# Performance work log

Hardware: AMD Instinct MI355X
Metric: run time of the kernel (lower is better)

## Reference

```python
import jax, jax.numpy as jnp
import numpy as np

N_NODES = 50000
N_EDGES = 800000
IN_DIM = 128
HIDDEN = 128
NUM_CLASSES = 2
NUM_GRAPHS = 512


def _linear_params(key, fan_in, fan_out):
    # torch nn.Linear default init: U(-1/sqrt(fan_in), 1/sqrt(fan_in))
    k1, k2 = jax.random.split(key)
    bound = 1.0 / np.sqrt(fan_in)
    W = jax.random.uniform(k1, (fan_in, fan_out), jnp.float32, -bound, bound)
    b = jax.random.uniform(k2, (fan_out,), jnp.float32, -bound, bound)
    return W, b


def setup_inputs() -> dict:
    key = jax.random.key(0)
    ks = jax.random.split(key, 8)
    x = jax.random.normal(ks[0], (N_NODES, IN_DIM), jnp.float32)
    edge_index = jax.random.randint(ks[1], (2, N_EDGES), 0, N_NODES, jnp.int64)
    batch = jnp.sort(jax.random.randint(ks[2], (N_NODES,), 0, NUM_GRAPHS, jnp.int64))
    W1a, b1a = _linear_params(ks[3], IN_DIM, HIDDEN)
    W1b, b1b = _linear_params(ks[4], HIDDEN, HIDDEN)
    W2a, b2a = _linear_params(ks[5], HIDDEN, HIDDEN)
    W2b, b2b = _linear_params(ks[6], HIDDEN, HIDDEN)
    Wfc, bfc = _linear_params(ks[7], HIDDEN, NUM_CLASSES)
    return {"x": x, "edge_index": edge_index, "batch": batch,
            "W1a": W1a, "b1a": b1a, "W1b": W1b, "b1b": b1b,
            "W2a": W2a, "b2a": b2a, "W2b": W2b, "b2b": b2b,
            "Wfc": Wfc, "bfc": bfc}


def _gin_layer(x, src, dst, Wa, ba, Wb, bb):
    # GINConv (eps=0): h_i = MLP(x_i + sum_{j->i} x_j)
    agg = jax.ops.segment_sum(x[src], dst, num_segments=N_NODES)
    h = x + agg
    h = jax.nn.relu(h @ Wa + ba)
    h = h @ Wb + bb
    return jax.nn.relu(h)  # outer F.relu in forward; dropout is identity (eval)


def reference(x, edge_index, batch, W1a, b1a, W1b, b1b, W2a, b2a, W2b, b2b, Wfc, bfc):
    src, dst = edge_index[0], edge_index[1]
    h = _gin_layer(x, src, dst, W1a, b1a, W1b, b1b)
    h = _gin_layer(h, src, dst, W2a, b2a, W2b, b2b)
    # global mean pool per graph
    sums = jax.ops.segment_sum(h, batch, num_segments=NUM_GRAPHS)
    counts = jax.ops.segment_sum(jnp.ones((N_NODES,), h.dtype), batch, num_segments=NUM_GRAPHS)
    g_emb = sums / jnp.maximum(counts, 1.0)[:, None]
    return g_emb @ Wfc + bfc  # [NUM_GRAPHS, NUM_CLASSES]
```

## Files before the change

kernel.cpp:

```cpp
#include <hip/hip_runtime.h>

typedef unsigned short ushort_t;
typedef unsigned int uint_t;

typedef __bf16 bf16x8 __attribute__((ext_vector_type(8)));
typedef float f32x4 __attribute__((ext_vector_type(4)));

#define N_NODES 50000
#define N_EDGES 800000
#define DIM 128
#define NUM_GRAPHS 512
#define LDA 136

#define ELL_CAP 64

#define EDGE_BLOCKS ((N_EDGES + 255) / 256)
#define PREP_X_BLOCKS 6250
#define PREP_W_BLOCKS 256
#define PREP_B_BLOCKS 196
#define PREP_TOTAL (EDGE_BLOCKS + PREP_X_BLOCKS + PREP_W_BLOCKS + PREP_B_BLOCKS + 1)

__device__ __forceinline__ float bf2f(ushort_t u) {
    return __uint_as_float(((uint_t)u) << 16);
}
__device__ __forceinline__ ushort_t f2bf(float f) {
    uint_t u = __float_as_uint(f);
    u = (u + 0x7FFF + ((u >> 16) & 1)) >> 16;
    return (ushort_t)u;
}
__device__ __forceinline__ bf16x8 as_bf16x8(uint4 v) {
    return __builtin_bit_cast(bf16x8, v);
}

__global__ void zero_detect_kernel(int* cnt, float* gsum, const void* xraw,
                                   const void* eiraw, int* flags) {
    int i = blockIdx.x * 256 + threadIdx.x;
    if (i < N_NODES) cnt[i] = 0;
    if (i < NUM_GRAPHS * DIM) gsum[i] = 0.f;
    if (i == 0) {
        const ushort_t* u = (const ushort_t*)xraw;
        int extreme = 0;
        for (int k = 0; k < 128; ++k) {
            int e = (u[k] >> 7) & 0xFF;
            if (e >= 0xC0) extreme++;
        }
        flags[0] = (extreme > 8) ? 1 : 0;
        const int* p = (const int*)eiraw;
        int nonzero = 0;
        for (int k = 1; k < 64; k += 2) nonzero += (p[k] != 0);
        flags[1] = (nonzero == 0) ? 1 : 0;
    }
}

__global__ __launch_bounds__(256) void prep_all_kernel(
    const void* xraw, const void* braw, const void* eiraw,
    const void* W0, const void* W1, const void* W2, const void* W3,
    const void* pb1a, const void* pb1b, const void* pb2a, const void* pb2b,
    const void* pWfc, const void* pbfc, const int* __restrict__ flags,
    ushort_t* __restrict__ xout, ushort_t* __restrict__ wpout,
    int* __restrict__ batch32, float* __restrict__ params,
    int* __restrict__ cnt, int* __restrict__ ell) {
    int b = blockIdx.x;
    int tid = threadIdx.x;
    if (b < EDGE_BLOCKS) {
        int e = b * 256 + tid;
        if (e < N_EDGES) {
            const int* p = (const int*)eiraw;
            int s, d;
            if (flags[1]) {
                s = p[2 * e];
                d = p[2 * (N_EDGES + e)];
            } else {
                s = p[e];
                d = p[N_EDGES + e];
            }
            int slot = atomicAdd(&cnt[d], 1);
            if (slot < ELL_CAP) ell[d * ELL_CAP + slot] = s;
        }
    } else if (b < EDGE_BLOCKS + PREP_X_BLOCKS) {
        int i = (b - EDGE_BLOCKS) * 256 + tid;
        if (i < N_NODES * DIM / 4) {
            if (flags[0]) {
                float4 v = ((const float4*)xraw)[i];
                ushort4 o;
                o.x = f2bf(v.x); o.y = f2bf(v.y); o.z = f2bf(v.z); o.w = f2bf(v.w);
                ((ushort4*)xout)[i] = o;
            } else {
                ((uint2*)xout)[i] = ((const uint2*)xraw)[i];
            }
        }
    } else if (b < EDGE_BLOCKS + PREP_X_BLOCKS + PREP_W_BLOCKS) {
        int gidx = (b - EDGE_BLOCKS - PREP_X_BLOCKS) * 256 + tid;
        int which = gidx >> 14;
        const void* W = (which == 0) ? W0 : (which == 1) ? W1 : (which == 2) ? W2 : W3;
        int idx = gidx & 16383;
        int j = idx & 7;
        int L = (idx >> 3) & 63;
        int t = (idx >> 9) & 7;
        int s = idx >> 12;
        int k = s * 32 + (L >> 4) * 8 + j;
        int n = t * 16 + (L & 15);
        int off = k * DIM + n;
        wpout[gidx] = flags[0] ? f2bf(((const float*)W)[off]) : ((const ushort_t*)W)[off];
    } else if (b < EDGE_BLOCKS + PREP_X_BLOCKS + PREP_W_BLOCKS + PREP_B_BLOCKS) {
        int i = (b - EDGE_BLOCKS - PREP_X_BLOCKS - PREP_W_BLOCKS) * 256 + tid;
        if (i < N_NODES) {
            const int* p = (const int*)braw;
            batch32[i] = flags[1] ? p[2 * i] : p[i];
        }
    } else {
        for (int i = tid; i < 770; i += 256) {
            const void* srcp;
            int j;
            if (i < 128)      { srcp = pb1a; j = i; }
            else if (i < 256) { srcp = pb1b; j = i - 128; }
            else if (i < 384) { srcp = pb2a; j = i - 256; }
            else if (i < 512) { srcp = pb2b; j = i - 384; }
            else if (i < 768) { srcp = pWfc; j = i - 512; }
            else              { srcp = pbfc; j = i - 768; }
            params[i] = flags[0] ? ((const float*)srcp)[j] : bf2f(((const ushort_t*)srcp)[j]);
        }
    }
}

__global__ __launch_bounds__(256) void agg_kernel(const ushort_t* __restrict__ feat,
                                                  const int* __restrict__ deg,
                                                  const int* __restrict__ ell,
                                                  ushort_t* __restrict__ hout) {
    int n = blockIdx.x * 16 + (threadIdx.x >> 4);
    int lane = threadIdx.x & 15;
    if (n >= N_NODES) return;
    const uint4* fp = reinterpret_cast<const uint4*>(feat);
    uint4 v = fp[(size_t)n * 16 + lane];
    float a0 = bf2f((ushort_t)(v.x & 0xffff));
    float a1 = bf2f((ushort_t)(v.x >> 16));
    float a2 = bf2f((ushort_t)(v.y & 0xffff));
    float a3 = bf2f((ushort_t)(v.y >> 16));
    float a4 = bf2f((ushort_t)(v.z & 0xffff));
    float a5 = bf2f((ushort_t)(v.z >> 16));
    float a6 = bf2f((ushort_t)(v.w & 0xffff));
    float a7 = bf2f((ushort_t)(v.w >> 16));
    int e1 = deg[n];
    if (e1 > ELL_CAP) e1 = ELL_CAP;
    const int* __restrict__ row = ell + (size_t)n * ELL_CAP;
    int j = 0;
#define ACC8(V) \
    a0 += bf2f((ushort_t)((V).x & 0xffff)); a1 += bf2f((ushort_t)((V).x >> 16)); \
    a2 += bf2f((ushort_t)((V).y & 0xffff)); a3 += bf2f((ushort_t)((V).y >> 16)); \
    a4 += bf2f((ushort_t)((V).z & 0xffff)); a5 += bf2f((ushort_t)((V).z >> 16)); \
    a6 += bf2f((ushort_t)((V).w & 0xffff)); a7 += bf2f((ushort_t)((V).w >> 16));
    for (; j + 8 <= e1; j += 8) {
        int s0 = row[j],     s1 = row[j + 1], s2 = row[j + 2], s3 = row[j + 3];
        int s4 = row[j + 4], s5 = row[j + 5], s6 = row[j + 6], s7 = row[j + 7];
        uint4 g0 = fp[(size_t)s0 * 16 + lane];
        uint4 g1 = fp[(size_t)s1 * 16 + lane];
        uint4 g2 = fp[(size_t)s2 * 16 + lane];
        uint4 g3 = fp[(size_t)s3 * 16 + lane];
        uint4 g4 = fp[(size_t)s4 * 16 + lane];
        uint4 g5 = fp[(size_t)s5 * 16 + lane];
        uint4 g6 = fp[(size_t)s6 * 16 + lane];
        uint4 g7 = fp[(size_t)s7 * 16 + lane];
        ACC8(g0) ACC8(g1) ACC8(g2) ACC8(g3)
        ACC8(g4) ACC8(g5) ACC8(g6) ACC8(g7)
    }
    for (; j + 4 <= e1; j += 4) {
        int s0 = row[j], s1 = row[j + 1], s2 = row[j + 2], s3 = row[j + 3];
        uint4 g0 = fp[(size_t)s0 * 16 + lane];
        uint4 g1 = fp[(size_t)s1 * 16 + lane];
        uint4 g2 = fp[(size_t)s2 * 16 + lane];
        uint4 g3 = fp[(size_t)s3 * 16 + lane];
        ACC8(g0) ACC8(g1) ACC8(g2) ACC8(g3)
    }
    for (; j < e1; ++j) {
        int s = row[j];
        uint4 g0 = fp[(size_t)s * 16 + lane];
        ACC8(g0)
    }
#undef ACC8
    uint4 o;
    o.x = (uint_t)f2bf(a0) | ((uint_t)f2bf(a1) << 16);
    o.y = (uint_t)f2bf(a2) | ((uint_t)f2bf(a3) << 16);
    o.z = (uint_t)f2bf(a4) | ((uint_t)f2bf(a5) << 16);
    o.w = (uint_t)f2bf(a6) | ((uint_t)f2bf(a7) << 16);
    reinterpret_cast<uint4*>(hout)[(size_t)n * 16 + lane] = o;
}

__global__ __launch_bounds__(256) void mlp_kernel(const ushort_t* __restrict__ hin,
                                                  const ushort_t* __restrict__ wpA,
                                                  const float* __restrict__ ba,
                                                  const ushort_t* __restrict__ wpB,
                                                  const float* __restrict__ bb,
                                                  ushort_t* __restrict__ hout) {
    __shared__ ushort_t As[64 * LDA];
    int tid = threadIdx.x;
    int wave = tid >> 6;
    int lane = tid & 63;
    int quad = lane >> 4;
    int cl = lane & 15;
    int row0 = blockIdx.x * 64;

    bf16x8 B1[2][4], B2[2][4];
#pragma unroll
    for (int ti = 0; ti < 2; ++ti) {
        int t = 2 * wave + ti;
#pragma unroll
        for (int s = 0; s < 4; ++s) {
            B1[ti][s] = as_bf16x8(reinterpret_cast<const uint4*>(wpA)[(s * 8 + t) * 64 + lane]);
            B2[ti][s] = as_bf16x8(reinterpret_cast<const uint4*>(wpB)[(s * 8 + t) * 64 + lane]);
        }
    }

    for (int i = tid; i < 64 * 16; i += 256) {
        int r = i >> 4, c8 = i & 15;
        uint4 v = make_uint4(0u, 0u, 0u, 0u);
        int gr = row0 + r;
        if (gr < N_NODES)
            v = reinterpret_cast<const uint4*>(hin + (size_t)gr * DIM)[c8];
        *reinterpret_cast<uint4*>(&As[r * LDA + c8 * 8]) = v;
    }
    __syncthreads();

    f32x4 acc[4][2];
#pragma unroll
    for (int m = 0; m < 4; ++m)
#pragma unroll
        for (int ti = 0; ti < 2; ++ti)
#pragma unroll
            for (int r = 0; r < 4; ++r) acc[m][ti][r] = 0.f;

#pragma unroll
    for (int s = 0; s < 4; ++s) {
#pragma unroll
        for (int m = 0; m < 4; ++m) {
            bf16x8 a = *reinterpret_cast<const bf16x8*>(&As[(m * 16 + cl) * LDA + s * 32 + quad * 8]);
#pragma unroll
            for (int ti = 0; ti < 2; ++ti)
                acc[m][ti] = __builtin_amdgcn_mfma_f32_16x16x32_bf16(a, B1[ti][s], acc[m][ti], 0, 0, 0);
        }
    }
    __syncthreads();

#pragma unroll
    for (int ti = 0; ti < 2; ++ti) {
        int col = 32 * wave + ti * 16 + cl;
        float bv = ba[col];
#pragma unroll
        for (int m = 0; m < 4; ++m)
#pragma unroll
            for (int r = 0; r < 4; ++r) {
                float v = acc[m][ti][r] + bv;
                As[(m * 16 + quad * 4 + r) * LDA + col] = f2bf(fmaxf(v, 0.f));
            }
    }
    __syncthreads();

#pragma unroll
    for (int m = 0; m < 4; ++m)
#pragma unroll
        for (int ti = 0; ti < 2; ++ti)
#pragma unroll
            for (int r = 0; r < 4; ++r) acc[m][ti][r] = 0.f;

#pragma unroll
    for (int s = 0; s < 4; ++s) {
#pragma unroll
        for (int m = 0; m < 4; ++m) {
            bf16x8 a = *reinterpret_cast<const bf16x8*>(&As[(m * 16 + cl) * LDA + s * 32 + quad * 8]);
#pragma unroll
            for (int ti = 0; ti < 2; ++ti)
                acc[m][ti] = __builtin_amdgcn_mfma_f32_16x16x32_bf16(a, B2[ti][s], acc[m][ti], 0, 0, 0);
        }
    }

#pragma unroll
    for (int ti = 0; ti < 2; ++ti) {
        int col = 32 * wave + ti * 16 + cl;
        float bv = bb[col];
#pragma unroll
        for (int m = 0; m < 4; ++m)
#pragma unroll
            for (int r = 0; r < 4; ++r) {
                int gr = row0 + m * 16 + quad * 4 + r;
                if (gr < N_NODES) {
                    float v = acc[m][ti][r] + bv;
                    hout[(size_t)gr * DIM + col] = f2bf(fmaxf(v, 0.f));
                }
            }
    }
}

__global__ __launch_bounds__(256) void mlp_pool_kernel(const ushort_t* __restrict__ hin,
                                                       const ushort_t* __restrict__ wpA,
                                                       const float* __restrict__ ba,
                                                       const ushort_t* __restrict__ wpB,
                                                       const float* __restrict__ bb,
                                                       const int* __restrict__ batch32,
                                                       float* __restrict__ gsum) {
    __shared__ ushort_t As[64 * LDA];
    int tid = threadIdx.x;
    int wave = tid >> 6;
    int lane = tid & 63;
    int quad = lane >> 4;
    int cl = lane & 15;
    int row0 = blockIdx.x * 64;

    bf16x8 B1[2][4], B2[2][4];
#pragma unroll
    for (int ti = 0; ti < 2; ++ti) {
        int t = 2 * wave + ti;
#pragma unroll
        for (int s = 0; s < 4; ++s) {
            B1[ti][s] = as_bf16x8(reinterpret_cast<const uint4*>(wpA)[(s * 8 + t) * 64 + lane]);
            B2[ti][s] = as_bf16x8(reinterpret_cast<const uint4*>(wpB)[(s * 8 + t) * 64 + lane]);
        }
    }

    for (int i = tid; i < 64 * 16; i += 256) {
        int r = i >> 4, c8 = i & 15;
        uint4 v = make_uint4(0u, 0u, 0u, 0u);
        int gr = row0 + r;
        if (gr < N_NODES)
            v = reinterpret_cast<const uint4*>(hin + (size_t)gr * DIM)[c8];
        *reinterpret_cast<uint4*>(&As[r * LDA + c8 * 8]) = v;
    }
    __syncthreads();

    f32x4 acc[4][2];
#pragma unroll
    for (int m = 0; m < 4; ++m)
#pragma unroll
        for (int ti = 0; ti < 2; ++ti)
#pragma unroll
            for (int r = 0; r < 4; ++r) acc[m][ti][r] = 0.f;

#pragma unroll
    for (int s = 0; s < 4; ++s) {
#pragma unroll
        for (int m = 0; m < 4; ++m) {
            bf16x8 a = *reinterpret_cast<const bf16x8*>(&As[(m * 16 + cl) * LDA + s * 32 + quad * 8]);
#pragma unroll
            for (int ti = 0; ti < 2; ++ti)
                acc[m][ti] = __builtin_amdgcn_mfma_f32_16x16x32_bf16(a, B1[ti][s], acc[m][ti], 0, 0, 0);
        }
    }
    __syncthreads();

#pragma unroll
    for (int ti = 0; ti < 2; ++ti) {
        int col = 32 * wave + ti * 16 + cl;
        float bv = ba[col];
#pragma unroll
        for (int m = 0; m < 4; ++m)
#pragma unroll
            for (int r = 0; r < 4; ++r) {
                float v = acc[m][ti][r] + bv;
                As[(m * 16 + quad * 4 + r) * LDA + col] = f2bf(fmaxf(v, 0.f));
            }
    }
    __syncthreads();

#pragma unroll
    for (int m = 0; m < 4; ++m)
#pragma unroll
        for (int ti = 0; ti < 2; ++ti)
#pragma unroll
            for (int r = 0; r < 4; ++r) acc[m][ti][r] = 0.f;

#pragma unroll
    for (int s = 0; s < 4; ++s) {
#pragma unroll
        for (int m = 0; m < 4; ++m) {
            bf16x8 a = *reinterpret_cast<const bf16x8*>(&As[(m * 16 + cl) * LDA + s * 32 + quad * 8]);
#pragma unroll
            for (int ti = 0; ti < 2; ++ti)
                acc[m][ti] = __builtin_amdgcn_mfma_f32_16x16x32_bf16(a, B2[ti][s], acc[m][ti], 0, 0, 0);
        }
    }
    __syncthreads();

#pragma unroll
    for (int ti = 0; ti < 2; ++ti) {
        int col = 32 * wave + ti * 16 + cl;
        float bv = bb[col];
#pragma unroll
        for (int m = 0; m < 4; ++m)
#pragma unroll
            for (int r = 0; r < 4; ++r) {
                float v = acc[m][ti][r] + bv;
                As[(m * 16 + quad * 4 + r) * LDA + col] = f2bf(fmaxf(v, 0.f));
            }
    }
    __syncthreads();

    int c = tid & 127;
    int rbase = (tid >> 7) * 32;
    float accp = 0.f;
    int curg = -1;
    for (int r = rbase; r < rbase + 32; ++r) {
        int gr = row0 + r;
        if (gr >= N_NODES) break;
        int g = batch32[gr];
        if (g != curg) {
            if (curg >= 0) atomicAdd(&gsum[curg * DIM + c], accp);
            curg = g;
            accp = 0.f;
        }
        accp += bf2f(As[r * LDA + c]);
    }
    if (curg >= 0) atomicAdd(&gsum[curg * DIM + c], accp);
}

__global__ __launch_bounds__(64) void fc_kernel(const float* __restrict__ gsum,
                                                const int* __restrict__ batch,
                                                const float* __restrict__ params,
                                                const int* __restrict__ flags,
                                                void* __restrict__ out) {
    int g = blockIdx.x;
    int l = threadIdx.x;
    int lo = 0, hi = N_NODES;
    while (lo < hi) { int mid = (lo + hi) >> 1; if (batch[mid] < g) lo = mid + 1; else hi = mid; }
    int start = lo;
    hi = N_NODES;
    while (lo < hi) { int mid = (lo + hi) >> 1; if (batch[mid] < g + 1) lo = mid + 1; else hi = mid; }
    int cnt = lo - start;
    float inv = 1.0f / (float)(cnt > 0 ? cnt : 1);
    float m0 = gsum[g * DIM + l] * inv;
    float m1 = gsum[g * DIM + 64 + l] * inv;
    float p0 = m0 * params[512 + l * 2 + 0] + m1 * params[512 + (64 + l) * 2 + 0];
    float p1 = m0 * params[512 + l * 2 + 1] + m1 * params[512 + (64 + l) * 2 + 1];
#pragma unroll
    for (int off = 32; off > 0; off >>= 1) {
        p0 += __shfl_down(p0, off, 64);
        p1 += __shfl_down(p1, off, 64);
    }
    if (l == 0) {
        float o0 = p0 + params[768];
        float o1 = p1 + params[769];
        if (flags[0]) {
            ((float*)out)[g * 2 + 0] = o0;
            ((float*)out)[g * 2 + 1] = o1;
        } else {
            ((ushort_t*)out)[g * 2 + 0] = f2bf(o0);
            ((ushort_t*)out)[g * 2 + 1] = f2bf(o1);
        }
    }
}

extern "C" void kernel_launch(void* const* d_in, const int* in_sizes, int n_in,
                              void* d_out, int out_size, void* d_ws, size_t ws_size,
                              hipStream_t stream) {
    const void* x = d_in[0];
    const void* ei = d_in[1];
    const void* batch = d_in[2];
    const void* W1a = d_in[3];
    const void* b1a = d_in[4];
    const void* W1b = d_in[5];
    const void* b1b = d_in[6];
    const void* W2a = d_in[7];
    const void* b2a = d_in[8];
    const void* W2b = d_in[9];
    const void* b2b = d_in[10];
    const void* Wfc = d_in[11];
    const void* bfc = d_in[12];

    char* base = (char*)d_ws;
    ushort_t* hX = (ushort_t*)base;   base += (size_t)N_NODES * DIM * 2;
    ushort_t* hA = (ushort_t*)base;   base += (size_t)N_NODES * DIM * 2;
    int* ell = (int*)base;            base += (size_t)N_NODES * ELL_CAP * 4;
    int* cnt = (int*)base;            base += (size_t)N_NODES * 4;
    int* batch32 = (int*)base;        base += (size_t)N_NODES * 4;
    ushort_t* wp = (ushort_t*)base;   base += 4 * 16384 * 2;
    float* params = (float*)base;     base += 772 * 4;
    float* gsum = (float*)base;       base += (size_t)NUM_GRAPHS * DIM * 4;
    int* flags = (int*)base;          base += 16;

    ushort_t* wpA1 = wp;
    ushort_t* wpB1 = wp + 16384;
    ushort_t* wpA2 = wp + 2 * 16384;
    ushort_t* wpB2 = wp + 3 * 16384;

    zero_detect_kernel<<<256, 256, 0, stream>>>(cnt, gsum, x, ei, flags);
    prep_all_kernel<<<PREP_TOTAL, 256, 0, stream>>>(x, batch, ei, W1a, W1b, W2a, W2b,
                                                    b1a, b1b, b2a, b2b, Wfc, bfc, flags,
                                                    hX, wp, batch32, params, cnt, ell);

    agg_kernel<<<(N_NODES + 15) / 16, 256, 0, stream>>>(hX, cnt, ell, hA);
    mlp_kernel<<<(N_NODES + 63) / 64, 256, 0, stream>>>(hA, wpA1, params + 0, wpB1, params + 128, hA);
    agg_kernel<<<(N_NODES + 15) / 16, 256, 0, stream>>>(hA, cnt, ell, hX);
    mlp_pool_kernel<<<(N_NODES + 63) / 64, 256, 0, stream>>>(hX, wpA2, params + 256, wpB2, params + 384,
                                                             batch32, gsum);
    fc_kernel<<<NUM_GRAPHS, 64, 0, stream>>>(gsum, batch32, params, flags, d_out);
}
```

Measured before the change: 245.1 us.

## Fuse neighbor aggregation into MLP kernels and bucket edge scatter by destination

The separate aggregation kernels are removed; each MLP block now gathers and sums neighbor rows for its 64 nodes straight into shared memory, so the aggregated features no longer make a round trip through global memory. Edge-to-ELL construction is split into 8 destination buckets, with each block scanning a 2048-edge chunk and keeping only destinations in its range. This is meant to improve atomic and write locality, at the cost of reading the edge list 8 times. The bf16 input copy is skipped by reading the raw input directly when it is already bf16. The trade-off is that gather latency now sits inside the GEMM blocks, and there are fewer threads per node during the gather.

```diff
diff --git a/kernel.cpp b/kernel.cpp
--- a/kernel.cpp
+++ b/kernel.cpp
@@ -14,7 +14,12 @@
 
 #define ELL_CAP 64
 
-#define EDGE_BLOCKS ((N_EDGES + 255) / 256)
+#define EDGE_GROUPS 8
+#define EDGE_BUCKET ((N_NODES + EDGE_GROUPS - 1) / EDGE_GROUPS)
+#define EDGE_CHUNK 2048
+#define EDGE_CHUNKS ((N_EDGES + EDGE_CHUNK - 1) / EDGE_CHUNK)
+#define EDGE_BLOCKS (EDGE_CHUNKS * EDGE_GROUPS)
+
 #define PREP_X_BLOCKS 6250
 #define PREP_W_BLOCKS 256
 #define PREP_B_BLOCKS 196
@@ -63,30 +68,32 @@
     int b = blockIdx.x;
     int tid = threadIdx.x;
     if (b < EDGE_BLOCKS) {
-        int e = b * 256 + tid;
-        if (e < N_EDGES) {
-            const int* p = (const int*)eiraw;
-            int s, d;
-            if (flags[1]) {
-                s = p[2 * e];
-                d = p[2 * (N_EDGES + e)];
-            } else {
-                s = p[e];
-                d = p[N_EDGES + e];
+        int group = b & (EDGE_GROUPS - 1);
+        int chunk = b >> 3;
+        int lo = group * EDGE_BUCKET;
+        int hi = lo + EDGE_BUCKET;
+        const int* p = (const int*)eiraw;
+        int i64 = flags[1];
+#pragma unroll
+        for (int i = 0; i < EDGE_CHUNK; i += 256) {
+            int e = chunk * EDGE_CHUNK + i + tid;
+            if (e < N_EDGES) {
+                int d = i64 ? p[2 * (N_EDGES + e)] : p[N_EDGES + e];
+                if (d >= lo && d < hi) {
+                    int s = i64 ? p[2 * e] : p[e];
+                    int slot = atomicAdd(&cnt[d], 1);
+                    if (slot < ELL_CAP) ell[d * ELL_CAP + slot] = s;
+                }
             }
-            int slot = atomicAdd(&cnt[d], 1);
-            if (slot < ELL_CAP) ell[d * ELL_CAP + slot] = s;
         }
     } else if (b < EDGE_BLOCKS + PREP_X_BLOCKS) {
-        int i = (b - EDGE_BLOCKS) * 256 + tid;
-        if (i < N_NODES * DIM / 4) {
-            if (flags[0]) {
+        if (flags[0]) {
+            int i = (b - EDGE_BLOCKS) * 256 + tid;
+            if (i < N_NODES * DIM / 4) {
                 float4 v = ((const float4*)xraw)[i];
                 ushort4 o;
                 o.x = f2bf(v.x); o.y = f2bf(v.y); o.z = f2bf(v.z); o.w = f2bf(v.w);
                 ((ushort4*)xout)[i] = o;
-            } else {
-                ((uint2*)xout)[i] = ((const uint2*)xraw)[i];
             }
         }
     } else if (b < EDGE_BLOCKS + PREP_X_BLOCKS + PREP_W_BLOCKS) {
@@ -123,14 +130,10 @@
     }
 }
 
-__global__ __launch_bounds__(256) void agg_kernel(const ushort_t* __restrict__ feat,
-                                                  const int* __restrict__ deg,
-                                                  const int* __restrict__ ell,
-                                                  ushort_t* __restrict__ hout) {
-    int n = blockIdx.x * 16 + (threadIdx.x >> 4);
-    int lane = threadIdx.x & 15;
-    if (n >= N_NODES) return;
-    const uint4* fp = reinterpret_cast<const uint4*>(feat);
+__device__ __forceinline__ uint4 gather_node_row(const uint4* __restrict__ fp,
+                                                 const int* __restrict__ deg,
+                                                 const int* __restrict__ ell,
+                                                 int n, int lane) {
     uint4 v = fp[(size_t)n * 16 + lane];
     float a0 = bf2f((ushort_t)(v.x & 0xffff));
     float a1 = bf2f((ushort_t)(v.x >> 16));
@@ -182,10 +185,31 @@
     o.y = (uint_t)f2bf(a2) | ((uint_t)f2bf(a3) << 16);
     o.z = (uint_t)f2bf(a4) | ((uint_t)f2bf(a5) << 16);
     o.w = (uint_t)f2bf(a6) | ((uint_t)f2bf(a7) << 16);
-    reinterpret_cast<uint4*>(hout)[(size_t)n * 16 + lane] = o;
-}
-
-__global__ __launch_bounds__(256) void mlp_kernel(const ushort_t* __restrict__ hin,
+    return o;
+}
+
+__device__ __forceinline__ void stage_gather(const ushort_t* feat,
+                                             const int* __restrict__ deg,
+                                             const int* __restrict__ ell,
+                                             int row0, int tid, ushort_t* As) {
+    const uint4* fp = reinterpret_cast<const uint4*>(feat);
+    int lane = tid & 15;
+    int sub = tid >> 4;
+#pragma unroll
+    for (int p = 0; p < 4; ++p) {
+        int r = p * 16 + sub;
+        int n = row0 + r;
+        uint4 o = make_uint4(0u, 0u, 0u, 0u);
+        if (n < N_NODES) o = gather_node_row(fp, deg, ell, n, lane);
+        *reinterpret_cast<uint4*>(&As[r * LDA + lane * 8]) = o;
+    }
+}
+
+__global__ __launch_bounds__(256) void mlp_kernel(const ushort_t* __restrict__ hX,
+                                                  const void* __restrict__ xraw,
+                                                  const int* __restrict__ flags,
+                                                  const int* __restrict__ deg,
+                                                  const int* __restrict__ ell,
                                                   const ushort_t* __restrict__ wpA,
                                                   const float* __restrict__ ba,
                                                   const ushort_t* __restrict__ wpB,
@@ -199,6 +223,9 @@
     int cl = lane & 15;
     int row0 = blockIdx.x * 64;
 
+    const ushort_t* feat = flags[0] ? hX : (const ushort_t*)xraw;
+    stage_gather(feat, deg, ell, row0, tid, As);
+
     bf16x8 B1[2][4], B2[2][4];
 #pragma unroll
     for (int ti = 0; ti < 2; ++ti) {
@@ -208,15 +235,6 @@
             B1[ti][s] = as_bf16x8(reinterpret_cast<const uint4*>(wpA)[(s * 8 + t) * 64 + lane]);
             B2[ti][s] = as_bf16x8(reinterpret_cast<const uint4*>(wpB)[(s * 8 + t) * 64 + lane]);
         }
-    }
-
-    for (int i = tid; i < 64 * 16; i += 256) {
-        int r = i >> 4, c8 = i & 15;
-        uint4 v = make_uint4(0u, 0u, 0u, 0u);
-        int gr = row0 + r;
-        if (gr < N_NODES)
-            v = reinterpret_cast<const uint4*>(hin + (size_t)gr * DIM)[c8];
-        *reinterpret_cast<uint4*>(&As[r * LDA + c8 * 8]) = v;
     }
     __syncthreads();
 
@@ -290,6 +308,8 @@
 }
 
 __global__ __launch_bounds__(256) void mlp_pool_kernel(const ushort_t* __restrict__ hin,
+                                                       const int* __restrict__ deg,
+                                                       const int* __restrict__ ell,
                                                        const ushort_t* __restrict__ wpA,
                                                        const float* __restrict__ ba,
                                                        const ushort_t* __restrict__ wpB,
@@ -304,6 +324,8 @@
     int cl = lane & 15;
     int row0 = blockIdx.x * 64;
 
+    stage_gather(hin, deg, ell, row0, tid, As);
+
     bf16x8 B1[2][4], B2[2][4];
 #pragma unroll
     for (int ti = 0; ti < 2; ++ti) {
@@ -313,15 +335,6 @@
             B1[ti][s] = as_bf16x8(reinterpret_cast<const uint4*>(wpA)[(s * 8 + t) * 64 + lane]);
             B2[ti][s] = as_bf16x8(reinterpret_cast<const uint4*>(wpB)[(s * 8 + t) * 64 + lane]);
         }
-    }
-
-    for (int i = tid; i < 64 * 16; i += 256) {
-        int r = i >> 4, c8 = i & 15;
-        uint4 v = make_uint4(0u, 0u, 0u, 0u);
-        int gr = row0 + r;
-        if (gr < N_NODES)
-            v = reinterpret_cast<const uint4*>(hin + (size_t)gr * DIM)[c8];
-        *reinterpret_cast<uint4*>(&As[r * LDA + c8 * 8]) = v;
     }
     __syncthreads();
 
@@ -484,10 +497,10 @@
                                                     b1a, b1b, b2a, b2b, Wfc, bfc, flags,
                                                     hX, wp, batch32, params, cnt, ell);
 
-    agg_kernel<<<(N_NODES + 15) / 16, 256, 0, stream>>>(hX, cnt, ell, hA);
-    mlp_kernel<<<(N_NODES + 63) / 64, 256, 0, stream>>>(hA, wpA1, params + 0, wpB1, params + 128, hA);
-    agg_kernel<<<(N_NODES + 15) / 16, 256, 0, stream>>>(hA, cnt, ell, hX);
-    mlp_pool_kernel<<<(N_NODES + 63) / 64, 256, 0, stream>>>(hX, wpA2, params + 256, wpB2, params + 384,
+    mlp_kernel<<<(N_NODES + 63) / 64, 256, 0, stream>>>(hX, x, flags, cnt, ell,
+                                                        wpA1, params + 0, wpB1, params + 128, hA);
+    mlp_pool_kernel<<<(N_NODES + 63) / 64, 256, 0, stream>>>(hA, cnt, ell,
+                                                             wpA2, params + 256, wpB2, params + 384,
                                                              batch32, gsum);
     fc_kernel<<<NUM_GRAPHS, 64, 0, stream>>>(gsum, batch32, params, flags, d_out);
 }
```

Result: slower. 253.7 us (+3.5%).
